# Kernel tuning notes

Hardware: AMD Instinct MI355X
Metric: run time of the kernel (lower is better)

The kernel has to match this reference:

```python
import jax, jax.numpy as jnp
import numpy as np

B, T, C, D = 256, 128, 141, 1536  # batch, tokens, max chars, feature dim
H = 141                            # lstm hidden
G = 4 * H                          # gate dim
L = 4                              # lstm layers


def setup_inputs() -> dict:
    key = jax.random.key(0)
    ks = jax.random.split(key, 20)
    s = 0.05
    tok_feats = jax.random.normal(ks[0], (B, T, D), jnp.float32)
    # non-overlapping char spans per token, clipped to C (some zero-length)
    lens = jax.random.randint(ks[1], (B, T), 0, 3)
    ends = jnp.cumsum(lens, axis=1)
    starts = ends - lens
    offset_mapping = jnp.stack([jnp.minimum(starts, C), jnp.minimum(ends, C)], axis=-1).astype(jnp.int32)
    return {
        "tok_feats": tok_feats,
        "offset_mapping": offset_mapping,
        "h0": jnp.zeros((2 * L, B, H), jnp.float32),
        "c0": jnp.zeros((2 * L, B, H), jnp.float32),
        "w_lin": jax.random.normal(ks[2], (D, D), jnp.float32) * s,
        "b_lin": jnp.zeros((D,), jnp.float32),
        "w_ih0_f": jax.random.normal(ks[3], (G, D), jnp.float32) * s,
        "w_ih0_b": jax.random.normal(ks[4], (G, D), jnp.float32) * s,
        "w_ih_f": jax.random.normal(ks[5], (L - 1, G, 2 * H), jnp.float32) * s,
        "w_ih_b": jax.random.normal(ks[6], (L - 1, G, 2 * H), jnp.float32) * s,
        "w_hh_f": jax.random.normal(ks[7], (L, G, H), jnp.float32) * s,
        "w_hh_b": jax.random.normal(ks[8], (L, G, H), jnp.float32) * s,
        "b_f": jnp.zeros((L, G), jnp.float32),
        "b_b": jnp.zeros((L, G), jnp.float32),
        "w1": jax.random.normal(ks[9], (2 * H, 2 * H), jnp.float32) * s,
        "b1": jnp.zeros((2 * H,), jnp.float32),
        "w2": jax.random.normal(ks[10], (2, 2 * H), jnp.float32) * s,
        "b2": jnp.zeros((2,), jnp.float32),
    }


def _scatter_chars(X, offset_mapping):
    # Vectorized equivalent of: for each token, write its vector into chars [start,end)
    starts = offset_mapping[..., 0]  # [B,T]
    ends = offset_mapping[..., 1]
    c = jnp.arange(C)
    cover = (starts[:, :, None] <= c) & (c < ends[:, :, None])  # [B,T,C]
    tok_idx = jnp.argmax(cover, axis=1)                          # [B,C]
    has = jnp.any(cover, axis=1)                                 # [B,C]
    chars = jnp.take_along_axis(X, tok_idx[:, :, None], axis=1)  # [B,C,D]
    return jnp.where(has[:, :, None], chars, jnp.zeros((), X.dtype))


def _run_dir(x, h_init, c_init, w_ih, w_hh, b, reverse):
    # x: [B,S,in]; precompute input contribution [S,B,4H]
    xW = jnp.swapaxes(jnp.einsum('bsd,gd->bsg', x, w_ih) + b, 0, 1)

    def step(carry, xt):
        h, cc = carry
        g = xt + h @ w_hh.T
        i = jax.nn.sigmoid(g[:, :H])
        f = jax.nn.sigmoid(g[:, H:2 * H])
        gg = jnp.tanh(g[:, 2 * H:3 * H])
        o = jax.nn.sigmoid(g[:, 3 * H:])
        c2 = f * cc + i * gg
        h2 = o * jnp.tanh(c2)
        return (h2, c2), h2

    (hn, cn), ys = jax.lax.scan(step, (h_init, c_init), xW, reverse=reverse)
    return jnp.swapaxes(ys, 0, 1), hn, cn  # [B,S,H]


def reference(tok_feats, offset_mapping, h0, c0, w_lin, b_lin,
              w_ih0_f, w_ih0_b, w_ih_f, w_ih_b, w_hh_f, w_hh_b, b_f, b_b,
              w1, b1, w2, b2):
    X = tok_feats @ w_lin.T + b_lin            # token-level linear (dropout is identity at eval)
    x = _scatter_chars(X, offset_mapping)      # [B,141,1536]
    h_list, c_list = [], []
    for l in range(L):
        wi_f = w_ih0_f if l == 0 else w_ih_f[l - 1]
        wi_b = w_ih0_b if l == 0 else w_ih_b[l - 1]
        out_f, hf, cf = _run_dir(x, h0[2 * l], c0[2 * l], wi_f, w_hh_f[l], b_f[l], False)
        out_b, hb, cb = _run_dir(x, h0[2 * l + 1], c0[2 * l + 1], wi_b, w_hh_b[l], b_b[l], True)
        x = jnp.concatenate([out_f, out_b], axis=-1)  # [B,141,282]
        h_list += [hf, hb]
        c_list += [cf, cb]
    hn = jnp.stack(h_list)
    cn = jnp.stack(c_list)
    y = x @ w1.T + b1
    y = y @ w2.T + b2                          # [B,141,2]
    X1, X2 = y[..., :1], y[..., 1:]
    return (X1, X2, hn, cn)
```

## Files before the change

### kernel.cpp

```cpp
#include <hip/hip_runtime.h>
#include <hip/hip_bf16.h>

#define Bb 256
#define Tt 128
#define Cc 141
#define Dd 1536
#define Hh 141
#define Gg 564
#define Gp 576
#define K2 288
#define NY 320
#define MM (Bb*Cc)

typedef float f32x4 __attribute__((ext_vector_type(4)));
typedef short s16x8 __attribute__((ext_vector_type(8)));
typedef _Float16 h2 __attribute__((ext_vector_type(2)));

__device__ __forceinline__ short f2bf(float f){
    union { float f; unsigned u; } v; v.f = f;
    unsigned r = v.u + 0x7fffu + ((v.u >> 16) & 1u);
    return (short)(r >> 16);
}
__device__ __forceinline__ float bf2f(short s){
    union { unsigned u; float f; } v; v.u = ((unsigned)(unsigned short)s) << 16;
    return v.f;
}
__device__ __forceinline__ float fdot2(h2 a, h2 b, float c){
#if __has_builtin(__builtin_amdgcn_fdot2)
    return __builtin_amdgcn_fdot2(a, b, c, false);
#else
    return c + (float)a.x * (float)b.x + (float)a.y * (float)b.y;
#endif
}
__device__ __forceinline__ float sigm(float x){ return 1.f / (1.f + __expf(-x)); }
__device__ __forceinline__ float tanh_(float x){ float e = __expf(2.f * x); return 1.f - 2.f / (e + 1.f); }

__global__ __launch_bounds__(256) void convert_pad(const float* __restrict__ src,
                                                   short* __restrict__ dst,
                                                   int R, int Kin, int Rp, int Kp){
    int idx = blockIdx.x * 256 + threadIdx.x;
    if (idx >= Rp * Kp) return;
    int r = idx / Kp, k = idx - r * Kp;
    float v = (r < R && k < Kin) ? src[(size_t)r * Kin + k] : 0.f;
    dst[idx] = f2bf(v);
}

__global__ __launch_bounds__(256) void build_gather(const int* __restrict__ offm,
                                                    int* __restrict__ gidx){
    int m = blockIdx.x * 256 + threadIdx.x;
    if (m >= MM) return;
    int b = m / Cc, c = m - b * Cc;
    int found = -1;
    for (int t = 0; t < Tt; t++){
        int s = offm[((size_t)(b * Tt + t)) * 2];
        int e = offm[((size_t)(b * Tt + t)) * 2 + 1];
        if (s <= c && c < e){ found = b * Tt + t; break; }
    }
    gidx[m] = found;
}

template<bool GATHER>
__global__ __launch_bounds__(256, 2) void gemm_bt(const void* __restrict__ Av,
                                                  const short* __restrict__ Bw,
                                                  const float* __restrict__ bias, int Nbias,
                                                  short* __restrict__ Cout,
                                                  const int* __restrict__ gidx,
                                                  int N, int K, int ldc){
    const int m0 = blockIdx.x * 128, n0 = blockIdx.y * 64;
    const int tid = threadIdx.x, lane = tid & 63, wid = tid >> 6;
    const int wm = wid >> 1, wn = wid & 1;
    __shared__ short As[128][40];
    __shared__ short Bs[64][40];
    f32x4 acc[4][2] = {};

    for (int k0 = 0; k0 < K; k0 += 32){
        if (!GATHER){
            const short* A = (const short*)Av;
            #pragma unroll
            for (int i = 0; i < 2; i++){
                int e = tid + i * 256;
                int row = e >> 2, c8 = e & 3;
                uint4 v = *(const uint4*)(A + (size_t)(m0 + row) * K + k0 + c8 * 8);
                *(uint4*)&As[row][c8 * 8] = v;
            }
        } else {
            const float* A = (const float*)Av;
            #pragma unroll
            for (int i = 0; i < 2; i++){
                int e = tid + i * 256;
                int row = e >> 2, c8 = e & 3;
                int g = gidx[m0 + row];
                uint4 pk = make_uint4(0u, 0u, 0u, 0u);
                if (g >= 0){
                    const float* src = A + (size_t)g * K + k0 + c8 * 8;
                    unsigned w0 = (unsigned short)f2bf(src[0]) | ((unsigned)(unsigned short)f2bf(src[1]) << 16);
                    unsigned w1 = (unsigned short)f2bf(src[2]) | ((unsigned)(unsigned short)f2bf(src[3]) << 16);
                    unsigned w2_ = (unsigned short)f2bf(src[4]) | ((unsigned)(unsigned short)f2bf(src[5]) << 16);
                    unsigned w3 = (unsigned short)f2bf(src[6]) | ((unsigned)(unsigned short)f2bf(src[7]) << 16);
                    pk = make_uint4(w0, w1, w2_, w3);
                }
                *(uint4*)&As[row][c8 * 8] = pk;
            }
        }
        {
            int row = tid >> 2, c8 = tid & 3;
            uint4 v = *(const uint4*)(Bw + (size_t)(n0 + row) * K + k0 + c8 * 8);
            *(uint4*)&Bs[row][c8 * 8] = v;
        }
        __syncthreads();

        const int kq = (lane >> 4) * 8, r16 = lane & 15;
        s16x8 af[4], bf[2];
        #pragma unroll
        for (int mt = 0; mt < 4; mt++) af[mt] = *(const s16x8*)&As[wm * 64 + mt * 16 + r16][kq];
        #pragma unroll
        for (int nt = 0; nt < 2; nt++) bf[nt] = *(const s16x8*)&Bs[wn * 32 + nt * 16 + r16][kq];
        #pragma unroll
        for (int mt = 0; mt < 4; mt++)
            #pragma unroll
            for (int nt = 0; nt < 2; nt++)
                acc[mt][nt] = __builtin_amdgcn_mfma_f32_16x16x32_bf16(af[mt], bf[nt], acc[mt][nt], 0, 0, 0);
        __syncthreads();
    }

    #pragma unroll
    for (int nt = 0; nt < 2; nt++){
        int col = n0 + wn * 32 + nt * 16 + (lane & 15);
        float bv = (col < Nbias) ? bias[col] : 0.f;
        #pragma unroll
        for (int mt = 0; mt < 4; mt++){
            int rowbase = m0 + wm * 64 + mt * 16 + (lane >> 4) * 4;
            #pragma unroll
            for (int r = 0; r < 4; r++){
                int row = rowbase + r;
                float v = acc[mt][nt][r] + bv;
                if (GATHER && gidx[row] < 0) v = 0.f;
                Cout[(size_t)row * ldc + col] = f2bf(v);
            }
        }
    }
}

__global__ __launch_bounds__(576) void lstm_scan(const short* __restrict__ xW_f,
                                                 const short* __restrict__ xW_b,
                                                 const float* __restrict__ whh_f,
                                                 const float* __restrict__ whh_b,
                                                 const float* __restrict__ h0l,
                                                 const float* __restrict__ c0l,
                                                 short* __restrict__ xout,
                                                 float* __restrict__ hnl,
                                                 float* __restrict__ cnl){
    const int dir = blockIdx.x & 1;
    const int b = blockIdx.x >> 1;
    const int j = threadIdx.x;
    const short* xW = dir ? xW_b : xW_f;
    const float* whh = dir ? whh_b : whh_f;

    __shared__ float pre[Gg];
    __shared__ h2 hsh[72];

    h2 wreg[71];
    if (j < Gg){
        const float* wr = whh + (size_t)j * Hh;
        #pragma unroll
        for (int kk = 0; kk < 70; kk++){
            h2 w; w.x = (_Float16)wr[2 * kk]; w.y = (_Float16)wr[2 * kk + 1];
            wreg[kk] = w;
        }
        h2 w; w.x = (_Float16)wr[140]; w.y = (_Float16)0.f;
        wreg[70] = w;
    }

    float hcur = 0.f, ccur = 0.f;
    if (j < Hh){
        hcur = h0l[(size_t)dir * Bb * Hh + b * Hh + j];
        ccur = c0l[(size_t)dir * Bb * Hh + b * Hh + j];
    }
    if (j < 144) ((_Float16*)hsh)[j] = (j < Hh) ? (_Float16)hcur : (_Float16)0.f;
    __syncthreads();

    for (int t = 0; t < Cc; t++){
        int tt = dir ? (Cc - 1 - t) : t;
        if (j < Gg){
            float xw = bf2f(xW[((size_t)b * Cc + tt) * Gp + j]);
            float acc0 = 0.f, acc1 = 0.f;
            #pragma unroll
            for (int kk = 0; kk < 71; kk++){
                if (kk & 1) acc1 = fdot2(wreg[kk], hsh[kk], acc1);
                else        acc0 = fdot2(wreg[kk], hsh[kk], acc0);
            }
            pre[j] = xw + acc0 + acc1;
        }
        __syncthreads();
        if (j < Hh){
            float gi = sigm(pre[j]);
            float gf = sigm(pre[j + Hh]);
            float gg = tanh_(pre[j + 2 * Hh]);
            float go = sigm(pre[j + 3 * Hh]);
            ccur = gf * ccur + gi * gg;
            hcur = go * tanh_(ccur);
            xout[((size_t)b * Cc + tt) * K2 + dir * Hh + j] = f2bf(hcur);
            ((_Float16*)hsh)[j] = (_Float16)hcur;
        }
        __syncthreads();
    }
    if (j < Hh){
        hnl[(size_t)dir * Bb * Hh + b * Hh + j] = hcur;
        cnl[(size_t)dir * Bb * Hh + b * Hh + j] = ccur;
    }
}

__global__ __launch_bounds__(256) void head2_k(const short* __restrict__ y1,
                                               const float* __restrict__ w2,
                                               const float* __restrict__ b2,
                                               float* __restrict__ X1,
                                               float* __restrict__ X2){
    int m = blockIdx.x * 256 + threadIdx.x;
    if (m >= MM) return;
    float a0 = b2[0], a1 = b2[1];
    for (int k = 0; k < 282; k++){
        float v = bf2f(y1[(size_t)m * NY + k]);
        a0 += v * w2[k];
        a1 += v * w2[282 + k];
    }
    X1[m] = a0;
    X2[m] = a1;
}

extern "C" void kernel_launch(void* const* d_in, const int* in_sizes, int n_in,
                              void* d_out, int out_size, void* d_ws, size_t ws_size,
                              hipStream_t stream){
    const float* tok     = (const float*)d_in[0];
    const int*   offm    = (const int*)d_in[1];
    const float* h0      = (const float*)d_in[2];
    const float* c0      = (const float*)d_in[3];
    const float* w_lin   = (const float*)d_in[4];
    const float* b_lin   = (const float*)d_in[5];
    const float* w_ih0_f = (const float*)d_in[6];
    const float* w_ih0_b = (const float*)d_in[7];
    const float* w_ih_f  = (const float*)d_in[8];
    const float* w_ih_b  = (const float*)d_in[9];
    const float* w_hh_f  = (const float*)d_in[10];
    const float* w_hh_b  = (const float*)d_in[11];
    const float* b_f     = (const float*)d_in[12];
    const float* b_b     = (const float*)d_in[13];
    const float* w1      = (const float*)d_in[14];
    const float* b1      = (const float*)d_in[15];
    const float* w2      = (const float*)d_in[16];
    const float* b2      = (const float*)d_in[17];

    float* out = (float*)d_out;
    float* oX1 = out;
    float* oX2 = out + MM;
    float* ohn = out + 2 * MM;
    float* ocn = ohn + 8 * Bb * Hh;

    char* ws = (char*)d_ws;
    size_t off = 0;
    auto alloc = [&](size_t bytes) -> void* {
        void* p = ws + off;
        off += (bytes + 255) & ~(size_t)255;
        return p;
    };
    short* x0      = (short*)alloc((size_t)MM * Dd * 2);
    short* wlin16  = (short*)alloc((size_t)Dd * Dd * 2);
    short* wih0f   = (short*)alloc((size_t)Gp * Dd * 2);
    short* wih0b   = (short*)alloc((size_t)Gp * Dd * 2);
    short* wihf123 = (short*)alloc((size_t)3 * Gp * K2 * 2);
    short* wihb123 = (short*)alloc((size_t)3 * Gp * K2 * 2);
    short* w1p     = (short*)alloc((size_t)NY * K2 * 2);
    int*   gidx    = (int*)alloc((size_t)MM * 4);
    short* xWf     = (short*)alloc((size_t)MM * Gp * 2);
    short* xWb     = (short*)alloc((size_t)MM * Gp * 2);
    short* xA      = (short*)alloc((size_t)MM * K2 * 2);
    short* xB      = (short*)alloc((size_t)MM * K2 * 2);
    short* y1      = xWf;

    auto cdiv = [](int a, int b){ return (a + b - 1) / b; };

    convert_pad<<<cdiv(Dd * Dd, 256), 256, 0, stream>>>(w_lin, wlin16, Dd, Dd, Dd, Dd);
    convert_pad<<<cdiv(Gp * Dd, 256), 256, 0, stream>>>(w_ih0_f, wih0f, Gg, Dd, Gp, Dd);
    convert_pad<<<cdiv(Gp * Dd, 256), 256, 0, stream>>>(w_ih0_b, wih0b, Gg, Dd, Gp, Dd);
    for (int l = 1; l < 4; l++){
        convert_pad<<<cdiv(Gp * K2, 256), 256, 0, stream>>>(w_ih_f + (size_t)(l - 1) * Gg * 282,
                                                            wihf123 + (size_t)(l - 1) * Gp * K2,
                                                            Gg, 282, Gp, K2);
        convert_pad<<<cdiv(Gp * K2, 256), 256, 0, stream>>>(w_ih_b + (size_t)(l - 1) * Gg * 282,
                                                            wihb123 + (size_t)(l - 1) * Gp * K2,
                                                            Gg, 282, Gp, K2);
    }
    convert_pad<<<cdiv(NY * K2, 256), 256, 0, stream>>>(w1, w1p, 282, 282, NY, K2);

    build_gather<<<cdiv(MM, 256), 256, 0, stream>>>(offm, gidx);
    hipMemsetAsync(xA, 0, (size_t)MM * K2 * 2, stream);
    hipMemsetAsync(xB, 0, (size_t)MM * K2 * 2, stream);

    gemm_bt<true><<<dim3(MM / 128, Dd / 64), 256, 0, stream>>>(tok, wlin16, b_lin, Dd, x0, gidx, Dd, Dd, Dd);

    const short* xin = x0;
    int Kl = Dd;
    short* outbuf[4] = { xA, xB, xA, xB };
    for (int l = 0; l < 4; l++){
        const short* wf = (l == 0) ? wih0f : wihf123 + (size_t)(l - 1) * Gp * K2;
        const short* wb = (l == 0) ? wih0b : wihb123 + (size_t)(l - 1) * Gp * K2;
        gemm_bt<false><<<dim3(MM / 128, Gp / 64), 256, 0, stream>>>(xin, wf, b_f + (size_t)l * Gg, Gg, xWf, nullptr, Gp, Kl, Gp);
        gemm_bt<false><<<dim3(MM / 128, Gp / 64), 256, 0, stream>>>(xin, wb, b_b + (size_t)l * Gg, Gg, xWb, nullptr, Gp, Kl, Gp);
        lstm_scan<<<512, 576, 0, stream>>>(xWf, xWb,
                                           w_hh_f + (size_t)l * Gg * Hh, w_hh_b + (size_t)l * Gg * Hh,
                                           h0 + (size_t)(2 * l) * Bb * Hh, c0 + (size_t)(2 * l) * Bb * Hh,
                                           outbuf[l],
                                           ohn + (size_t)(2 * l) * Bb * Hh, ocn + (size_t)(2 * l) * Bb * Hh);
        xin = outbuf[l];
        Kl = K2;
    }

    gemm_bt<false><<<dim3(MM / 128, NY / 64), 256, 0, stream>>>(xin, w1p, b1, 282, y1, nullptr, NY, K2, NY);
    head2_k<<<cdiv(MM, 256), 256, 0, stream>>>(y1, w2, b2, oX1, oX2);
}
```

Baseline: 2.474 ms.

## Replace GEMM with swizzled 128x128 LDS-DMA kernel, merge directions, fold head

Replaces the 128x64 GEMM with a 128x128-tile, K=64 kernel. It uses global_load_lds direct loads, an XOR-swizzled shared-memory layout and an XCD-aware block remapping. The fp32 gather and bf16 conversion move into a separate gather_convert pass. Forward and backward input projections are merged into one GEMM with N=1152, and the w1/w2 head is folded into a single combined weight vector applied per row. The zeroing memsets are dropped and buffers are aliased, so the padded K columns now hold stale but finite data that meets zero-padded weights.

```diff
diff --git a/kernel.cpp b/kernel.cpp
--- a/kernel.cpp
+++ b/kernel.cpp
@@ -8,13 +8,17 @@
 #define Hh 141
 #define Gg 564
 #define Gp 576
-#define K2 288
-#define NY 320
+#define Nc 1152
+#define K2p 320
 #define MM (Bb*Cc)
 
 typedef float f32x4 __attribute__((ext_vector_type(4)));
 typedef short s16x8 __attribute__((ext_vector_type(8)));
 typedef _Float16 h2 __attribute__((ext_vector_type(2)));
+
+typedef __attribute__((address_space(1))) const void GvT;
+typedef __attribute__((address_space(3))) void LvT;
+#define GLOAD16(g, l) __builtin_amdgcn_global_load_lds((GvT*)(g), (LvT*)(l), 16, 0, 0)
 
 __device__ __forceinline__ short f2bf(float f){
     union { float f; unsigned u; } v; v.f = f;
@@ -59,90 +63,109 @@
     gidx[m] = found;
 }
 
-template<bool GATHER>
-__global__ __launch_bounds__(256, 2) void gemm_bt(const void* __restrict__ Av,
+__global__ __launch_bounds__(256) void gather_convert(const float* __restrict__ tok,
+                                                      const int* __restrict__ gidx,
+                                                      short* __restrict__ xg){
+    size_t idx = (size_t)blockIdx.x * 256 + threadIdx.x;
+    if (idx >= (size_t)MM * 192) return;
+    int m = (int)(idx / 192), c8 = (int)(idx % 192);
+    int g = gidx[m];
+    s16x8 o = (s16x8)0;
+    if (g >= 0){
+        const float* s = tok + (size_t)g * Dd + c8 * 8;
+        float4 v0 = *(const float4*)s;
+        float4 v1 = *(const float4*)(s + 4);
+        o[0] = f2bf(v0.x); o[1] = f2bf(v0.y); o[2] = f2bf(v0.z); o[3] = f2bf(v0.w);
+        o[4] = f2bf(v1.x); o[5] = f2bf(v1.y); o[6] = f2bf(v1.z); o[7] = f2bf(v1.w);
+    }
+    *(s16x8*)(xg + (size_t)m * Dd + c8 * 8) = o;
+}
+
+__global__ __launch_bounds__(256, 2) void gemm128(const short* __restrict__ A,
                                                   const short* __restrict__ Bw,
-                                                  const float* __restrict__ bias, int Nbias,
+                                                  const float* __restrict__ bias1,
+                                                  const float* __restrict__ bias2,
+                                                  int nb1, int nb2, int halfN,
                                                   short* __restrict__ Cout,
                                                   const int* __restrict__ gidx,
-                                                  int N, int K, int ldc){
-    const int m0 = blockIdx.x * 128, n0 = blockIdx.y * 64;
-    const int tid = threadIdx.x, lane = tid & 63, wid = tid >> 6;
-    const int wm = wid >> 1, wn = wid & 1;
-    __shared__ short As[128][40];
-    __shared__ short Bs[64][40];
-    f32x4 acc[4][2] = {};
-
-    for (int k0 = 0; k0 < K; k0 += 32){
-        if (!GATHER){
-            const short* A = (const short*)Av;
-            #pragma unroll
-            for (int i = 0; i < 2; i++){
-                int e = tid + i * 256;
-                int row = e >> 2, c8 = e & 3;
-                uint4 v = *(const uint4*)(A + (size_t)(m0 + row) * K + k0 + c8 * 8);
-                *(uint4*)&As[row][c8 * 8] = v;
-            }
-        } else {
-            const float* A = (const float*)Av;
-            #pragma unroll
-            for (int i = 0; i < 2; i++){
-                int e = tid + i * 256;
-                int row = e >> 2, c8 = e & 3;
-                int g = gidx[m0 + row];
-                uint4 pk = make_uint4(0u, 0u, 0u, 0u);
-                if (g >= 0){
-                    const float* src = A + (size_t)g * K + k0 + c8 * 8;
-                    unsigned w0 = (unsigned short)f2bf(src[0]) | ((unsigned)(unsigned short)f2bf(src[1]) << 16);
-                    unsigned w1 = (unsigned short)f2bf(src[2]) | ((unsigned)(unsigned short)f2bf(src[3]) << 16);
-                    unsigned w2_ = (unsigned short)f2bf(src[4]) | ((unsigned)(unsigned short)f2bf(src[5]) << 16);
-                    unsigned w3 = (unsigned short)f2bf(src[6]) | ((unsigned)(unsigned short)f2bf(src[7]) << 16);
-                    pk = make_uint4(w0, w1, w2_, w3);
-                }
-                *(uint4*)&As[row][c8 * 8] = pk;
-            }
-        }
-        {
-            int row = tid >> 2, c8 = tid & 3;
-            uint4 v = *(const uint4*)(Bw + (size_t)(n0 + row) * K + k0 + c8 * 8);
-            *(uint4*)&Bs[row][c8 * 8] = v;
+                                                  int K, int NT, int ldc){
+    __shared__ short As[128 * 64];
+    __shared__ short Bs[128 * 64];
+    const int nwg = gridDim.x;
+    const int id = blockIdx.x;
+    const int q = nwg >> 3, r = nwg & 7;
+    const int xcd = id & 7, pos = id >> 3;
+    const int wg = (xcd < r ? xcd * (q + 1) : r * (q + 1) + (xcd - r) * q) + pos;
+    const int m0 = (wg / NT) * 128, n0 = (wg % NT) * 128;
+    const int tid = threadIdx.x, lane = tid & 63, wv = tid >> 6;
+    const int wm = wv >> 1, wn = wv & 1;
+    const int r16 = lane & 15, kq = lane >> 4;
+
+    f32x4 acc[4][4] = {};
+
+    for (int k0 = 0; k0 < K; k0 += 64){
+        #pragma unroll
+        for (int i = 0; i < 4; i++){
+            int e = (i * 4 + wv) * 64 + lane;
+            int row = e >> 3, ch = e & 7;
+            int sc = ch ^ (row & 7);
+            GLOAD16(A + (size_t)(m0 + row) * K + k0 + (sc << 3),
+                    As + (i * 4 + wv) * 512);
+        }
+        #pragma unroll
+        for (int i = 0; i < 4; i++){
+            int e = (i * 4 + wv) * 64 + lane;
+            int row = e >> 3, ch = e & 7;
+            int sc = ch ^ (row & 7);
+            GLOAD16(Bw + (size_t)(n0 + row) * K + k0 + (sc << 3),
+                    Bs + (i * 4 + wv) * 512);
         }
         __syncthreads();
-
-        const int kq = (lane >> 4) * 8, r16 = lane & 15;
-        s16x8 af[4], bf[2];
-        #pragma unroll
-        for (int mt = 0; mt < 4; mt++) af[mt] = *(const s16x8*)&As[wm * 64 + mt * 16 + r16][kq];
-        #pragma unroll
-        for (int nt = 0; nt < 2; nt++) bf[nt] = *(const s16x8*)&Bs[wn * 32 + nt * 16 + r16][kq];
-        #pragma unroll
-        for (int mt = 0; mt < 4; mt++)
-            #pragma unroll
-            for (int nt = 0; nt < 2; nt++)
-                acc[mt][nt] = __builtin_amdgcn_mfma_f32_16x16x32_bf16(af[mt], bf[nt], acc[mt][nt], 0, 0, 0);
+        #pragma unroll
+        for (int ks = 0; ks < 2; ks++){
+            s16x8 af[4], bfr[4];
+            #pragma unroll
+            for (int mt = 0; mt < 4; mt++){
+                int row = wm * 64 + mt * 16 + r16;
+                int c = (ks * 4 + kq) ^ (row & 7);
+                af[mt] = *(const s16x8*)(As + row * 64 + (c << 3));
+            }
+            #pragma unroll
+            for (int nt = 0; nt < 4; nt++){
+                int row = wn * 64 + nt * 16 + r16;
+                int c = (ks * 4 + kq) ^ (row & 7);
+                bfr[nt] = *(const s16x8*)(Bs + row * 64 + (c << 3));
+            }
+            #pragma unroll
+            for (int mt = 0; mt < 4; mt++)
+                #pragma unroll
+                for (int nt = 0; nt < 4; nt++)
+                    acc[mt][nt] = __builtin_amdgcn_mfma_f32_16x16x32_bf16(af[mt], bfr[nt], acc[mt][nt], 0, 0, 0);
+        }
         __syncthreads();
     }
 
     #pragma unroll
-    for (int nt = 0; nt < 2; nt++){
-        int col = n0 + wn * 32 + nt * 16 + (lane & 15);
-        float bv = (col < Nbias) ? bias[col] : 0.f;
+    for (int nt = 0; nt < 4; nt++){
+        int col = n0 + wn * 64 + nt * 16 + r16;
+        float bv;
+        if (col < halfN) bv = (col < nb1) ? bias1[col] : 0.f;
+        else             bv = (col - halfN < nb2) ? bias2[col - halfN] : 0.f;
         #pragma unroll
         for (int mt = 0; mt < 4; mt++){
-            int rowbase = m0 + wm * 64 + mt * 16 + (lane >> 4) * 4;
-            #pragma unroll
-            for (int r = 0; r < 4; r++){
-                int row = rowbase + r;
-                float v = acc[mt][nt][r] + bv;
-                if (GATHER && gidx[row] < 0) v = 0.f;
+            int rowb = m0 + wm * 64 + mt * 16 + kq * 4;
+            #pragma unroll
+            for (int rr = 0; rr < 4; rr++){
+                int row = rowb + rr;
+                float v = acc[mt][nt][rr] + bv;
+                if (gidx && gidx[row] < 0) v = 0.f;
                 Cout[(size_t)row * ldc + col] = f2bf(v);
             }
         }
     }
 }
 
-__global__ __launch_bounds__(576) void lstm_scan(const short* __restrict__ xW_f,
-                                                 const short* __restrict__ xW_b,
+__global__ __launch_bounds__(576) void lstm_scan(const short* __restrict__ xW,
                                                  const float* __restrict__ whh_f,
                                                  const float* __restrict__ whh_b,
                                                  const float* __restrict__ h0l,
@@ -153,7 +176,6 @@
     const int dir = blockIdx.x & 1;
     const int b = blockIdx.x >> 1;
     const int j = threadIdx.x;
-    const short* xW = dir ? xW_b : xW_f;
     const float* whh = dir ? whh_b : whh_f;
 
     __shared__ float pre[Gg];
@@ -182,7 +204,7 @@
     for (int t = 0; t < Cc; t++){
         int tt = dir ? (Cc - 1 - t) : t;
         if (j < Gg){
-            float xw = bf2f(xW[((size_t)b * Cc + tt) * Gp + j]);
+            float xw = bf2f(xW[((size_t)b * Cc + tt) * Nc + dir * Gp + j]);
             float acc0 = 0.f, acc1 = 0.f;
             #pragma unroll
             for (int kk = 0; kk < 71; kk++){
@@ -199,7 +221,7 @@
             float go = sigm(pre[j + 3 * Hh]);
             ccur = gf * ccur + gi * gg;
             hcur = go * tanh_(ccur);
-            xout[((size_t)b * Cc + tt) * K2 + dir * Hh + j] = f2bf(hcur);
+            xout[((size_t)b * Cc + tt) * K2p + dir * Hh + j] = f2bf(hcur);
             ((_Float16*)hsh)[j] = (_Float16)hcur;
         }
         __syncthreads();
@@ -210,21 +232,51 @@
     }
 }
 
-__global__ __launch_bounds__(256) void head2_k(const short* __restrict__ y1,
-                                               const float* __restrict__ w2,
-                                               const float* __restrict__ b2,
+__global__ __launch_bounds__(384) void wc_build(const float* __restrict__ w1,
+                                                const float* __restrict__ b1,
+                                                const float* __restrict__ w2,
+                                                const float* __restrict__ b2,
+                                                float* __restrict__ Wc){
+    int j = threadIdx.x;
+    if (j < K2p){
+        float a0 = 0.f, a1 = 0.f;
+        if (j < 282){
+            for (int k = 0; k < 282; k++){
+                float w = w1[(size_t)k * 282 + j];
+                a0 += w2[k] * w;
+                a1 += w2[282 + k] * w;
+            }
+        }
+        Wc[j] = a0;
+        Wc[K2p + j] = a1;
+    } else if (j < K2p + 2){
+        int o = j - K2p;
+        float s = b2[o];
+        for (int k = 0; k < 282; k++) s += w2[(size_t)o * 282 + k] * b1[k];
+        Wc[2 * K2p + o] = s;
+    }
+}
+
+__global__ __launch_bounds__(256) void head2_k(const short* __restrict__ x4,
+                                               const float* __restrict__ Wc,
                                                float* __restrict__ X1,
                                                float* __restrict__ X2){
     int m = blockIdx.x * 256 + threadIdx.x;
     if (m >= MM) return;
-    float a0 = b2[0], a1 = b2[1];
-    for (int k = 0; k < 282; k++){
-        float v = bf2f(y1[(size_t)m * NY + k]);
-        a0 += v * w2[k];
-        a1 += v * w2[282 + k];
-    }
-    X1[m] = a0;
-    X2[m] = a1;
+    const short* xr = x4 + (size_t)m * K2p;
+    float a0 = 0.f, a1 = 0.f;
+    #pragma unroll 4
+    for (int c = 0; c < 36; c++){
+        s16x8 v = *(const s16x8*)(xr + c * 8);
+        #pragma unroll
+        for (int u = 0; u < 8; u++){
+            float xv = bf2f(v[u]);
+            a0 += xv * Wc[c * 8 + u];
+            a1 += xv * Wc[K2p + c * 8 + u];
+        }
+    }
+    X1[m] = a0 + Wc[2 * K2p];
+    X2[m] = a1 + Wc[2 * K2p + 1];
 }
 
 extern "C" void kernel_launch(void* const* d_in, const int* in_sizes, int n_in,
@@ -262,58 +314,56 @@
         off += (bytes + 255) & ~(size_t)255;
         return p;
     };
-    short* x0      = (short*)alloc((size_t)MM * Dd * 2);
+    short* region1 = (short*)alloc((size_t)MM * Dd * 2);
+    short* region2 = (short*)alloc((size_t)MM * Dd * 2);
     short* wlin16  = (short*)alloc((size_t)Dd * Dd * 2);
-    short* wih0f   = (short*)alloc((size_t)Gp * Dd * 2);
-    short* wih0b   = (short*)alloc((size_t)Gp * Dd * 2);
-    short* wihf123 = (short*)alloc((size_t)3 * Gp * K2 * 2);
-    short* wihb123 = (short*)alloc((size_t)3 * Gp * K2 * 2);
-    short* w1p     = (short*)alloc((size_t)NY * K2 * 2);
+    short* w0c     = (short*)alloc((size_t)Nc * Dd * 2);
+    short* wc123   = (short*)alloc((size_t)3 * Nc * K2p * 2);
     int*   gidx    = (int*)alloc((size_t)MM * 4);
-    short* xWf     = (short*)alloc((size_t)MM * Gp * 2);
-    short* xWb     = (short*)alloc((size_t)MM * Gp * 2);
-    short* xA      = (short*)alloc((size_t)MM * K2 * 2);
-    short* xB      = (short*)alloc((size_t)MM * K2 * 2);
-    short* y1      = xWf;
+    float* Wc      = (float*)alloc((size_t)(2 * K2p + 2) * 4);
+
+    short* xg = region1;
+    short* xW = region1;
+    short* x0 = region2;
+    short* xA = region2;
+    short* xB = region2 + (size_t)MM * K2p;
 
     auto cdiv = [](int a, int b){ return (a + b - 1) / b; };
 
     convert_pad<<<cdiv(Dd * Dd, 256), 256, 0, stream>>>(w_lin, wlin16, Dd, Dd, Dd, Dd);
-    convert_pad<<<cdiv(Gp * Dd, 256), 256, 0, stream>>>(w_ih0_f, wih0f, Gg, Dd, Gp, Dd);
-    convert_pad<<<cdiv(Gp * Dd, 256), 256, 0, stream>>>(w_ih0_b, wih0b, Gg, Dd, Gp, Dd);
+    convert_pad<<<cdiv(Gp * Dd, 256), 256, 0, stream>>>(w_ih0_f, w0c, Gg, Dd, Gp, Dd);
+    convert_pad<<<cdiv(Gp * Dd, 256), 256, 0, stream>>>(w_ih0_b, w0c + (size_t)Gp * Dd, Gg, Dd, Gp, Dd);
     for (int l = 1; l < 4; l++){
-        convert_pad<<<cdiv(Gp * K2, 256), 256, 0, stream>>>(w_ih_f + (size_t)(l - 1) * Gg * 282,
-                                                            wihf123 + (size_t)(l - 1) * Gp * K2,
-                                                            Gg, 282, Gp, K2);
-        convert_pad<<<cdiv(Gp * K2, 256), 256, 0, stream>>>(w_ih_b + (size_t)(l - 1) * Gg * 282,
-                                                            wihb123 + (size_t)(l - 1) * Gp * K2,
-                                                            Gg, 282, Gp, K2);
-    }
-    convert_pad<<<cdiv(NY * K2, 256), 256, 0, stream>>>(w1, w1p, 282, 282, NY, K2);
+        short* wl = wc123 + (size_t)(l - 1) * Nc * K2p;
+        convert_pad<<<cdiv(Gp * K2p, 256), 256, 0, stream>>>(w_ih_f + (size_t)(l - 1) * Gg * 282,
+                                                             wl, Gg, 282, Gp, K2p);
+        convert_pad<<<cdiv(Gp * K2p, 256), 256, 0, stream>>>(w_ih_b + (size_t)(l - 1) * Gg * 282,
+                                                             wl + (size_t)Gp * K2p, Gg, 282, Gp, K2p);
+    }
+    wc_build<<<1, 384, 0, stream>>>(w1, b1, w2, b2, Wc);
 
     build_gather<<<cdiv(MM, 256), 256, 0, stream>>>(offm, gidx);
-    hipMemsetAsync(xA, 0, (size_t)MM * K2 * 2, stream);
-    hipMemsetAsync(xB, 0, (size_t)MM * K2 * 2, stream);
-
-    gemm_bt<true><<<dim3(MM / 128, Dd / 64), 256, 0, stream>>>(tok, wlin16, b_lin, Dd, x0, gidx, Dd, Dd, Dd);
+    gather_convert<<<cdiv(MM * 192, 256), 256, 0, stream>>>(tok, gidx, xg);
+
+    gemm128<<<282 * (Dd / 128), 256, 0, stream>>>(xg, wlin16, b_lin, b_lin,
+                                                  Dd, 0, Dd, x0, gidx, Dd, Dd / 128, Dd);
 
     const short* xin = x0;
     int Kl = Dd;
     short* outbuf[4] = { xA, xB, xA, xB };
     for (int l = 0; l < 4; l++){
-        const short* wf = (l == 0) ? wih0f : wihf123 + (size_t)(l - 1) * Gp * K2;
-        const short* wb = (l == 0) ? wih0b : wihb123 + (size_t)(l - 1) * Gp * K2;
-        gemm_bt<false><<<dim3(MM / 128, Gp / 64), 256, 0, stream>>>(xin, wf, b_f + (size_t)l * Gg, Gg, xWf, nullptr, Gp, Kl, Gp);
-        gemm_bt<false><<<dim3(MM / 128, Gp / 64), 256, 0, stream>>>(xin, wb, b_b + (size_t)l * Gg, Gg, xWb, nullptr, Gp, Kl, Gp);
-        lstm_scan<<<512, 576, 0, stream>>>(xWf, xWb,
+        const short* wl = (l == 0) ? w0c : wc123 + (size_t)(l - 1) * Nc * K2p;
+        gemm128<<<282 * (Nc / 128), 256, 0, stream>>>(xin, wl,
+                                                      b_f + (size_t)l * Gg, b_b + (size_t)l * Gg,
+                                                      Gg, Gg, Gp, xW, nullptr, Kl, Nc / 128, Nc);
+        lstm_scan<<<512, 576, 0, stream>>>(xW,
                                            w_hh_f + (size_t)l * Gg * Hh, w_hh_b + (size_t)l * Gg * Hh,
                                            h0 + (size_t)(2 * l) * Bb * Hh, c0 + (size_t)(2 * l) * Bb * Hh,
                                            outbuf[l],
                                            ohn + (size_t)(2 * l) * Bb * Hh, ocn + (size_t)(2 * l) * Bb * Hh);
         xin = outbuf[l];
-        Kl = K2;
-    }
-
-    gemm_bt<false><<<dim3(MM / 128, NY / 64), 256, 0, stream>>>(xin, w1p, b1, 282, y1, nullptr, NY, K2, NY);
-    head2_k<<<cdiv(MM, 256), 256, 0, stream>>>(y1, w2, b2, oX1, oX2);
-}
+        Kl = K2p;
+    }
+
+    head2_k<<<cdiv(MM, 256), 256, 0, stream>>>(xB, Wc, oX1, oX2);
+}
```

Result: faster. 2.036 ms (-17.7%).
